# Kernel tuning notes

Hardware: AMD Instinct MI355X
Metric: run time of the kernel (lower is better)

## Reference

```python
import jax, jax.numpy as jnp
import numpy as np
import math

B, S, E = 4, 1024, 1024
H = 16
HD = E // H            # 64
HD2 = HD // 2          # 32
DEPTH = 12 - 1
LAMBDA_INIT = 0.8 - 0.6 * math.exp(-0.3 * DEPTH)
EPS = 1e-5


def setup_inputs() -> dict:
    key = jax.random.key(0)
    ks = jax.random.split(key, 16)
    std = 1.0 / math.sqrt(E)
    inp = {
        "hidden_states": jax.random.normal(ks[0], (B, S, E), jnp.float32),
        "q_w": jax.random.normal(ks[1], (E, E), jnp.float32) * std,
        "q_b": jnp.zeros((E,), jnp.float32),
        "k_w": jax.random.normal(ks[2], (E, E), jnp.float32) * std,
        "k_b": jnp.zeros((E,), jnp.float32),
        "v_w": jax.random.normal(ks[3], (E, E), jnp.float32) * std,
        "v_b": jnp.zeros((E,), jnp.float32),
        "o_w": jax.random.normal(ks[4], (E, E), jnp.float32) * std,
        "o_b": jnp.zeros((E,), jnp.float32),
        "lambda_q1": jax.random.normal(ks[5], (HD2,), jnp.float32) * 0.1,
        "lambda_k1": jax.random.normal(ks[6], (HD2,), jnp.float32) * 0.1,
        "lambda_q2": jax.random.normal(ks[7], (HD2,), jnp.float32) * 0.1,
        "lambda_k2": jax.random.normal(ks[8], (HD2,), jnp.float32) * 0.1,
        "subln_w": jnp.ones((HD,), jnp.float32),
    }
    return inp


def reference(hidden_states, q_w, q_b, k_w, k_b, v_w, v_b, o_w, o_b,
              lambda_q1, lambda_k1, lambda_q2, lambda_k2, subln_w):
    b, s, _ = hidden_states.shape
    # projections (torch Linear: x @ W.T + b)
    q = hidden_states @ q_w.T + q_b
    k = hidden_states @ k_w.T + k_b
    v = hidden_states @ v_w.T + v_b
    # split q/k into 2*H heads of dim HD2; v into H heads of dim HD
    q = q.reshape(b, s, 2 * H, HD2).transpose(0, 2, 1, 3)   # [B,2H,S,HD2]
    k = k.reshape(b, s, 2 * H, HD2).transpose(0, 2, 1, 3)   # [B,2H,S,HD2]
    v = v.reshape(b, s, H, HD).transpose(0, 2, 1, 3)        # [B,H,S,HD]
    # scores scaled by sqrt(head_dim) (full head_dim, per source)
    scores = jnp.einsum('bhqd,bhkd->bhqk', q, k) / math.sqrt(HD)
    scores = jnp.nan_to_num(scores)
    attn_w = jax.nn.softmax(scores.astype(jnp.float32), axis=-1).astype(scores.dtype)
    lam1 = jnp.exp(jnp.sum(lambda_q1 * lambda_k1))
    lam2 = jnp.exp(jnp.sum(lambda_q2 * lambda_k2))
    lam = lam1 - lam2 + LAMBDA_INIT
    attn_w = attn_w.reshape(b, H, 2, s, s)
    diff_w = attn_w[:, :, 0] - lam * attn_w[:, :, 1]        # [B,H,S,S]
    attn = jnp.einsum('bhqk,bhkd->bhqd', diff_w, v)          # [B,H,S,HD]
    # RMSNorm over head dim, elementwise affine
    attn = attn * jax.lax.rsqrt(jnp.mean(attn * attn, axis=-1, keepdims=True) + EPS) * subln_w
    attn = attn * (1.0 - LAMBDA_INIT)
    attn = attn.transpose(0, 2, 1, 3).reshape(b, s, H * HD)
    out = attn @ o_w.T + o_b
    return out, diff_w
```

## Files before the change

### kernel.cpp

```cpp
#include <hip/hip_runtime.h>

typedef __attribute__((ext_vector_type(8))) short short8;
typedef __attribute__((ext_vector_type(4))) float floatx4;

#define MFMA16(a, b, c) __builtin_amdgcn_mfma_f32_16x16x32_bf16((a), (b), (c), 0, 0, 0)

#define LAMBDA_INIT_F 0.777870099559256f
#define ONE_MINUS_LAMBDA_F 0.222129900440744f

#define GLL(g, l)                                                              \
  __builtin_amdgcn_global_load_lds(                                            \
      (const __attribute__((address_space(1))) void*)(g),                      \
      (__attribute__((address_space(3))) void*)(l), 16, 0, 0)

static __device__ __forceinline__ unsigned short f2bf(float f) {
  union { float f; unsigned int u; } v; v.f = f;
  unsigned int r = v.u + 0x7FFFu + ((v.u >> 16) & 1u);
  return (unsigned short)(r >> 16);
}

__global__ __launch_bounds__(256) void cvt_f32_bf16(const float* __restrict__ in,
                                                    unsigned short* __restrict__ out,
                                                    int n4) {
  int i = blockIdx.x * 256 + threadIdx.x;
  if (i < n4) {
    float4 v = ((const float4*)in)[i];
    unsigned short o0 = f2bf(v.x), o1 = f2bf(v.y), o2 = f2bf(v.z), o3 = f2bf(v.w);
    ushort2 a = {o0, o1}, b = {o2, o3};
    ((ushort2*)out)[i * 2] = a;
    ((ushort2*)out)[i * 2 + 1] = b;
  }
}

__device__ __forceinline__ void gemm128_core(const unsigned short* __restrict__ A,
                                             const unsigned short* __restrict__ Bt,
                                             unsigned short* As, unsigned short* Bs,
                                             int m0, int n0, floatx4 (&acc)[4][4]) {
  const int tid = threadIdx.x;
  const int w = tid >> 6, lane = tid & 63;
  const int lrow = lane & 15, quad = lane >> 4;
  const int wm = (w >> 1) * 64, wn = (w & 1) * 64;

#pragma unroll
  for (int i = 0; i < 4; i++)
#pragma unroll
    for (int j = 0; j < 4; j++)
      acc[i][j] = (floatx4){0.f, 0.f, 0.f, 0.f};

  const int ar = tid >> 2;
  const int ac = (tid & 3) * 8;
  const unsigned short* ga = A + (size_t)(m0 + ar) * 1024 + ac;
  const unsigned short* gb = Bt + (size_t)(n0 + ar) * 1024 + ac;
  unsigned short* la = As + w * 512;
  unsigned short* lb = Bs + w * 512;

  for (int k0 = 0; k0 < 1024; k0 += 32) {
    GLL(ga + k0, la);
    GLL(ga + k0 + 64 * 1024, la + 2048);
    GLL(gb + k0, lb);
    GLL(gb + k0 + 64 * 1024, lb + 2048);
    __syncthreads();
    short8 af[4], bfr[4];
#pragma unroll
    for (int i = 0; i < 4; i++)
      af[i] = *(const short8*)(As + (wm + i * 16 + lrow) * 32 + quad * 8);
#pragma unroll
    for (int j = 0; j < 4; j++)
      bfr[j] = *(const short8*)(Bs + (wn + j * 16 + lrow) * 32 + quad * 8);
#pragma unroll
    for (int i = 0; i < 4; i++)
#pragma unroll
      for (int j = 0; j < 4; j++)
        acc[i][j] = MFMA16(af[i], bfr[j], acc[i][j]);
    __syncthreads();
  }
}

__global__ __launch_bounds__(256, 2) void gemm_qkv(const unsigned short* __restrict__ A,
                                                   const unsigned short* __restrict__ qw,
                                                   const unsigned short* __restrict__ kw,
                                                   const unsigned short* __restrict__ vw,
                                                   const float* __restrict__ qb,
                                                   const float* __restrict__ kb,
                                                   const float* __restrict__ vb,
                                                   unsigned short* __restrict__ qh,
                                                   unsigned short* __restrict__ kh,
                                                   unsigned short* __restrict__ vnat) {
  __shared__ unsigned short As[128 * 32];
  __shared__ unsigned short Bs[128 * 32];
  const int m0 = blockIdx.y * 128;
  const int nglob = blockIdx.x * 128;
  const int wsel = nglob >> 10;
  const int nloc = nglob & 1023;
  const unsigned short* Bt = (wsel == 0) ? qw : ((wsel == 1) ? kw : vw);
  const float* bias = (wsel == 0) ? qb : ((wsel == 1) ? kb : vb);

  floatx4 acc[4][4];
  gemm128_core(A, Bt, As, Bs, m0, nloc, acc);

  const int tid = threadIdx.x;
  const int w = tid >> 6, lane = tid & 63;
  const int lrow = lane & 15, quad = lane >> 4;
  const int wm = (w >> 1) * 64, wn = (w & 1) * 64;

#pragma unroll
  for (int i = 0; i < 4; i++)
#pragma unroll
    for (int j = 0; j < 4; j++) {
      int col = nloc + wn + j * 16 + lrow;
      float bcol = bias[col];
#pragma unroll
      for (int r = 0; r < 4; r++) {
        int row = m0 + wm + i * 16 + quad * 4 + r;
        float v = acc[i][j][r] + bcol;
        if (wsel < 2) {
          int b = row >> 10, s = row & 1023, h2 = col >> 5, d = col & 31;
          unsigned short* o = (wsel == 0) ? qh : kh;
          o[((((size_t)(b * 32 + h2)) << 10) + s) * 32 + d] = f2bf(v);
        } else {
          vnat[(size_t)row * 1024 + col] = f2bf(v);
        }
      }
    }
}

__global__ __launch_bounds__(256, 2) void gemm_o(const unsigned short* __restrict__ A,
                                                 const unsigned short* __restrict__ ow,
                                                 const float* __restrict__ ob,
                                                 float* __restrict__ out) {
  __shared__ unsigned short As[128 * 32];
  __shared__ unsigned short Bs[128 * 32];
  const int m0 = blockIdx.y * 128;
  const int n0 = blockIdx.x * 128;

  floatx4 acc[4][4];
  gemm128_core(A, ow, As, Bs, m0, n0, acc);

  const int tid = threadIdx.x;
  const int w = tid >> 6, lane = tid & 63;
  const int lrow = lane & 15, quad = lane >> 4;
  const int wm = (w >> 1) * 64, wn = (w & 1) * 64;

#pragma unroll
  for (int i = 0; i < 4; i++)
#pragma unroll
    for (int j = 0; j < 4; j++) {
      int col = n0 + wn + j * 16 + lrow;
      float bcol = ob[col];
#pragma unroll
      for (int r = 0; r < 4; r++) {
        int row = m0 + wm + i * 16 + quad * 4 + r;
        out[(size_t)row * 1024 + col] = acc[i][j][r] + bcol;
      }
    }
}

__global__ __launch_bounds__(256) void transpose_v(const unsigned short* __restrict__ vn,
                                                   unsigned short* __restrict__ vt) {
  __shared__ unsigned int tile[64][65];
  const int t = threadIdx.x;
  const int bh = blockIdx.y, b = bh >> 4, h = bh & 15;
  const int s0 = blockIdx.x * 64;
#pragma unroll
  for (int i = 0; i < 2; i++) {
    int r = i * 32 + (t >> 3);
    int c8 = (t & 7) * 8;
    short8 v = *(const short8*)(vn + ((size_t)(b * 1024 + s0 + r)) * 1024 + h * 64 + c8);
#pragma unroll
    for (int j = 0; j < 8; j++) tile[r][c8 + j] = (unsigned short)v[j];
  }
  __syncthreads();
  const int w = t >> 6, lane = t & 63;
#pragma unroll
  for (int dd = 0; dd < 16; dd++) {
    int d = w * 16 + dd;
    unsigned short u = (unsigned short)tile[lane][d];
    vt[(((size_t)(b * 16 + h)) * 64 + d) * 1024 + s0 + lane] = u;
  }
}

__global__ __launch_bounds__(256) void attn_fused(const unsigned short* __restrict__ qh,
                                                  const unsigned short* __restrict__ kh,
                                                  const unsigned short* __restrict__ vt,
                                                  const float* __restrict__ lq1,
                                                  const float* __restrict__ lk1,
                                                  const float* __restrict__ lq2,
                                                  const float* __restrict__ lk2,
                                                  const float* __restrict__ subln,
                                                  float* __restrict__ diffw,
                                                  unsigned short* __restrict__ attnb) {
  __shared__ float redm[4][2][16];
  __shared__ float redl[4][2][16];
  __shared__ unsigned short dsA[4][16][40];
  __shared__ float ored[4][16][64];

  const int tid = threadIdx.x;
  const int w = tid >> 6, lane = tid & 63;
  const int lrow = lane & 15, quad = lane >> 4;
  const int blk = blockIdx.x;
  const int chunk = blk & 63, bh = blk >> 6;
  const int b = bh >> 4, h = bh & 15;
  const int r0 = chunk * 16;
  const int cbase = w * 256;

  float sl1 = 0.f, sl2 = 0.f;
  for (int i = 0; i < 32; i++) { sl1 += lq1[i] * lk1[i]; sl2 += lq2[i] * lk2[i]; }
  const float lam = __expf(sl1) - __expf(sl2) + LAMBDA_INIT_F;

  const unsigned short* q1 = qh + ((((size_t)(b * 32 + 2 * h)) << 10) + r0) * 32;
  const unsigned short* q2 = q1 + (32u << 10);
  const unsigned short* k1 = kh + (((size_t)(b * 32 + 2 * h)) << 10) * 32;
  const unsigned short* k2 = k1 + (32u << 10);
  const unsigned short* vth = vt + (((size_t)(b * 16 + h)) << 16);

  short8 a1 = *(const short8*)(q1 + lrow * 32 + quad * 8);
  short8 a2 = *(const short8*)(q2 + lrow * 32 + quad * 8);

  floatx4 s1a[16], s2a[16];
  float m1[4], m2[4];
#pragma unroll
  for (int r = 0; r < 4; r++) { m1[r] = -1e30f; m2[r] = -1e30f; }

  const floatx4 zero = (floatx4){0.f, 0.f, 0.f, 0.f};

#pragma unroll
  for (int ct = 0; ct < 16; ct++) {
    short8 bk = *(const short8*)(k1 + (size_t)(cbase + ct * 16 + lrow) * 32 + quad * 8);
    floatx4 s = MFMA16(a1, bk, zero);
#pragma unroll
    for (int r = 0; r < 4; r++) {
      float v = s[r] * 0.125f;
      s1a[ct][r] = v;
      m1[r] = fmaxf(m1[r], v);
    }
  }
#pragma unroll
  for (int ct = 0; ct < 16; ct++) {
    short8 bk = *(const short8*)(k2 + (size_t)(cbase + ct * 16 + lrow) * 32 + quad * 8);
    floatx4 s = MFMA16(a2, bk, zero);
#pragma unroll
    for (int r = 0; r < 4; r++) {
      float v = s[r] * 0.125f;
      s2a[ct][r] = v;
      m2[r] = fmaxf(m2[r], v);
    }
  }

#pragma unroll
  for (int off = 1; off < 16; off <<= 1) {
#pragma unroll
    for (int r = 0; r < 4; r++) {
      m1[r] = fmaxf(m1[r], __shfl_xor(m1[r], off));
      m2[r] = fmaxf(m2[r], __shfl_xor(m2[r], off));
    }
  }
  if (lrow == 0) {
#pragma unroll
    for (int r = 0; r < 4; r++) {
      redm[w][0][quad * 4 + r] = m1[r];
      redm[w][1][quad * 4 + r] = m2[r];
    }
  }
  __syncthreads();
  float mf1[4], mf2[4];
#pragma unroll
  for (int r = 0; r < 4; r++) {
    int rr = quad * 4 + r;
    mf1[r] = fmaxf(fmaxf(redm[0][0][rr], redm[1][0][rr]), fmaxf(redm[2][0][rr], redm[3][0][rr]));
    mf2[r] = fmaxf(fmaxf(redm[0][1][rr], redm[1][1][rr]), fmaxf(redm[2][1][rr], redm[3][1][rr]));
  }

  float l1[4] = {0.f, 0.f, 0.f, 0.f}, l2[4] = {0.f, 0.f, 0.f, 0.f};
#pragma unroll
  for (int ct = 0; ct < 16; ct++) {
#pragma unroll
    for (int r = 0; r < 4; r++) {
      float e1 = __expf(s1a[ct][r] - mf1[r]);
      s1a[ct][r] = e1;
      l1[r] += e1;
      float e2 = __expf(s2a[ct][r] - mf2[r]);
      s2a[ct][r] = e2;
      l2[r] += e2;
    }
  }
#pragma unroll
  for (int off = 1; off < 16; off <<= 1) {
#pragma unroll
    for (int r = 0; r < 4; r++) {
      l1[r] += __shfl_xor(l1[r], off);
      l2[r] += __shfl_xor(l2[r], off);
    }
  }
  if (lrow == 0) {
#pragma unroll
    for (int r = 0; r < 4; r++) {
      redl[w][0][quad * 4 + r] = l1[r];
      redl[w][1][quad * 4 + r] = l2[r];
    }
  }
  __syncthreads();
  float il1[4], il2[4];
#pragma unroll
  for (int r = 0; r < 4; r++) {
    int rr = quad * 4 + r;
    il1[r] = 1.f / (redl[0][0][rr] + redl[1][0][rr] + redl[2][0][rr] + redl[3][0][rr]);
    il2[r] = 1.f / (redl[0][1][rr] + redl[1][1][rr] + redl[2][1][rr] + redl[3][1][rr]);
  }

  floatx4 accO[4];
#pragma unroll
  for (int nt = 0; nt < 4; nt++) accO[nt] = zero;

  float* dwbase = diffw + (((size_t)bh) << 20) + (size_t)r0 * 1024 + cbase;

#pragma unroll
  for (int c2 = 0; c2 < 8; c2++) {
#pragma unroll
    for (int cc = 0; cc < 2; cc++) {
      int ct = c2 * 2 + cc;
#pragma unroll
      for (int r = 0; r < 4; r++) {
        float p1 = s1a[ct][r] * il1[r];
        float p2 = s2a[ct][r] * il2[r];
        float d = p1 - lam * p2;
        dwbase[(size_t)(quad * 4 + r) * 1024 + ct * 16 + lrow] = d;
        dsA[w][quad * 4 + r][cc * 16 + lrow] = f2bf(d);
      }
    }
    short8 ad = *(const short8*)(&dsA[w][lrow][quad * 8]);
#pragma unroll
    for (int nt = 0; nt < 4; nt++) {
      short8 bv = *(const short8*)(vth + (size_t)(nt * 16 + lrow) * 1024 + cbase + c2 * 32 + quad * 8);
      accO[nt] = MFMA16(ad, bv, accO[nt]);
    }
  }

#pragma unroll
  for (int nt = 0; nt < 4; nt++)
#pragma unroll
    for (int r = 0; r < 4; r++)
      ored[w][quad * 4 + r][nt * 16 + lrow] = accO[nt][r];
  __syncthreads();

#pragma unroll
  for (int rr = 0; rr < 4; rr++) {
    int row = w * 4 + rr;
    float o = ored[0][row][lane] + ored[1][row][lane] + ored[2][row][lane] + ored[3][row][lane];
    float ss = o * o;
#pragma unroll
    for (int off = 1; off < 64; off <<= 1) ss += __shfl_xor(ss, off);
    float rs = rsqrtf(ss * (1.f / 64.f) + 1e-5f);
    float v = o * rs * subln[lane] * ONE_MINUS_LAMBDA_F;
    attnb[((((size_t)b) << 10) + r0 + row) * 1024 + h * 64 + lane] = f2bf(v);
  }
}

extern "C" void kernel_launch(void* const* d_in, const int* in_sizes, int n_in,
                              void* d_out, int out_size, void* d_ws, size_t ws_size,
                              hipStream_t stream) {
  (void)in_sizes; (void)n_in; (void)out_size; (void)ws_size;
  const float* hs = (const float*)d_in[0];
  const float* q_w = (const float*)d_in[1];
  const float* q_b = (const float*)d_in[2];
  const float* k_w = (const float*)d_in[3];
  const float* k_b = (const float*)d_in[4];
  const float* v_w = (const float*)d_in[5];
  const float* v_b = (const float*)d_in[6];
  const float* o_w = (const float*)d_in[7];
  const float* o_b = (const float*)d_in[8];
  const float* lq1 = (const float*)d_in[9];
  const float* lk1 = (const float*)d_in[10];
  const float* lq2 = (const float*)d_in[11];
  const float* lk2 = (const float*)d_in[12];
  const float* subln = (const float*)d_in[13];

  char* ws = (char*)d_ws;
  unsigned short* hs_bf = (unsigned short*)(ws + 0);
  unsigned short* attnb = (unsigned short*)(ws + 0);
  unsigned short* qw_bf = (unsigned short*)(ws + 8388608);
  unsigned short* kw_bf = (unsigned short*)(ws + 10485760);
  unsigned short* vw_bf = (unsigned short*)(ws + 12582912);
  unsigned short* ow_bf = (unsigned short*)(ws + 14680064);
  unsigned short* q_h = (unsigned short*)(ws + 16777216);
  unsigned short* k_h = (unsigned short*)(ws + 25165824);
  unsigned short* v_nat = (unsigned short*)(ws + 33554432);
  unsigned short* v_t = (unsigned short*)(ws + 41943040);

  cvt_f32_bf16<<<4096, 256, 0, stream>>>(hs, hs_bf, 1048576);
  cvt_f32_bf16<<<1024, 256, 0, stream>>>(q_w, qw_bf, 262144);
  cvt_f32_bf16<<<1024, 256, 0, stream>>>(k_w, kw_bf, 262144);
  cvt_f32_bf16<<<1024, 256, 0, stream>>>(v_w, vw_bf, 262144);
  cvt_f32_bf16<<<1024, 256, 0, stream>>>(o_w, ow_bf, 262144);

  gemm_qkv<<<dim3(24, 32), 256, 0, stream>>>(hs_bf, qw_bf, kw_bf, vw_bf,
                                             q_b, k_b, v_b, q_h, k_h, v_nat);

  transpose_v<<<dim3(16, 64), 256, 0, stream>>>(v_nat, v_t);

  float* outf = (float*)d_out;
  attn_fused<<<4096, 256, 0, stream>>>(q_h, k_h, v_t, lq1, lk1, lq2, lk2, subln,
                                       outf + 4194304, attnb);

  gemm_o<<<dim3(8, 32), 256, 0, stream>>>(attnb, ow_bf, o_b, outf);
}
```

Measured before the change: 531.5 us.

## Give each wave a full 16-row chunk and recompute scores instead of storing them

Each wavefront now owns a whole 16-row query chunk over all 1024 keys, which removes the cross-wave shared-memory reductions, barriers and the output reduction buffer. Softmax runs in two passes: the first accumulates exp sums without max subtraction, and the second recomputes QK^T with MFMA to produce normalized probabilities, so the 32 score registers per lane are no longer needed. The grid shrinks fourfold. In exchange the QK MFMAs and K loads are doubled, and dropping the max subtraction relies on scores staying small enough that exp does not overflow.

```diff
diff --git a/kernel.cpp b/kernel.cpp
--- a/kernel.cpp
+++ b/kernel.cpp
@@ -189,19 +189,15 @@
                                                   const float* __restrict__ subln,
                                                   float* __restrict__ diffw,
                                                   unsigned short* __restrict__ attnb) {
-  __shared__ float redm[4][2][16];
-  __shared__ float redl[4][2][16];
   __shared__ unsigned short dsA[4][16][40];
-  __shared__ float ored[4][16][64];
 
   const int tid = threadIdx.x;
   const int w = tid >> 6, lane = tid & 63;
   const int lrow = lane & 15, quad = lane >> 4;
-  const int blk = blockIdx.x;
-  const int chunk = blk & 63, bh = blk >> 6;
+  const int chunk = blockIdx.x * 4 + w;
+  const int cidx = chunk & 63, bh = chunk >> 6;
   const int b = bh >> 4, h = bh & 15;
-  const int r0 = chunk * 16;
-  const int cbase = w * 256;
+  const int r0 = cidx * 16;
 
   float sl1 = 0.f, sl2 = 0.f;
   for (int i = 0; i < 32; i++) { sl1 += lq1[i] * lk1[i]; sl2 += lq2[i] * lk2[i]; }
@@ -216,113 +212,55 @@
   short8 a1 = *(const short8*)(q1 + lrow * 32 + quad * 8);
   short8 a2 = *(const short8*)(q2 + lrow * 32 + quad * 8);
 
-  floatx4 s1a[16], s2a[16];
-  float m1[4], m2[4];
-#pragma unroll
-  for (int r = 0; r < 4; r++) { m1[r] = -1e30f; m2[r] = -1e30f; }
-
   const floatx4 zero = (floatx4){0.f, 0.f, 0.f, 0.f};
 
-#pragma unroll
-  for (int ct = 0; ct < 16; ct++) {
-    short8 bk = *(const short8*)(k1 + (size_t)(cbase + ct * 16 + lrow) * 32 + quad * 8);
-    floatx4 s = MFMA16(a1, bk, zero);
+  float sum1[4] = {0.f, 0.f, 0.f, 0.f}, sum2[4] = {0.f, 0.f, 0.f, 0.f};
+#pragma unroll 8
+  for (int ct = 0; ct < 64; ct++) {
+    short8 bk1 = *(const short8*)(k1 + (size_t)(ct * 16 + lrow) * 32 + quad * 8);
+    short8 bk2 = *(const short8*)(k2 + (size_t)(ct * 16 + lrow) * 32 + quad * 8);
+    floatx4 s1 = MFMA16(a1, bk1, zero);
+    floatx4 s2 = MFMA16(a2, bk2, zero);
 #pragma unroll
     for (int r = 0; r < 4; r++) {
-      float v = s[r] * 0.125f;
-      s1a[ct][r] = v;
-      m1[r] = fmaxf(m1[r], v);
-    }
-  }
-#pragma unroll
-  for (int ct = 0; ct < 16; ct++) {
-    short8 bk = *(const short8*)(k2 + (size_t)(cbase + ct * 16 + lrow) * 32 + quad * 8);
-    floatx4 s = MFMA16(a2, bk, zero);
+      sum1[r] += __expf(s1[r] * 0.125f);
+      sum2[r] += __expf(s2[r] * 0.125f);
+    }
+  }
+#pragma unroll
+  for (int off = 1; off < 16; off <<= 1)
 #pragma unroll
     for (int r = 0; r < 4; r++) {
-      float v = s[r] * 0.125f;
-      s2a[ct][r] = v;
-      m2[r] = fmaxf(m2[r], v);
-    }
-  }
-
-#pragma unroll
-  for (int off = 1; off < 16; off <<= 1) {
-#pragma unroll
-    for (int r = 0; r < 4; r++) {
-      m1[r] = fmaxf(m1[r], __shfl_xor(m1[r], off));
-      m2[r] = fmaxf(m2[r], __shfl_xor(m2[r], off));
-    }
-  }
-  if (lrow == 0) {
-#pragma unroll
-    for (int r = 0; r < 4; r++) {
-      redm[w][0][quad * 4 + r] = m1[r];
-      redm[w][1][quad * 4 + r] = m2[r];
-    }
-  }
-  __syncthreads();
-  float mf1[4], mf2[4];
+      sum1[r] += __shfl_xor(sum1[r], off);
+      sum2[r] += __shfl_xor(sum2[r], off);
+    }
+  float il1[4], il2[4];
 #pragma unroll
   for (int r = 0; r < 4; r++) {
-    int rr = quad * 4 + r;
-    mf1[r] = fmaxf(fmaxf(redm[0][0][rr], redm[1][0][rr]), fmaxf(redm[2][0][rr], redm[3][0][rr]));
-    mf2[r] = fmaxf(fmaxf(redm[0][1][rr], redm[1][1][rr]), fmaxf(redm[2][1][rr], redm[3][1][rr]));
-  }
-
-  float l1[4] = {0.f, 0.f, 0.f, 0.f}, l2[4] = {0.f, 0.f, 0.f, 0.f};
-#pragma unroll
-  for (int ct = 0; ct < 16; ct++) {
-#pragma unroll
-    for (int r = 0; r < 4; r++) {
-      float e1 = __expf(s1a[ct][r] - mf1[r]);
-      s1a[ct][r] = e1;
-      l1[r] += e1;
-      float e2 = __expf(s2a[ct][r] - mf2[r]);
-      s2a[ct][r] = e2;
-      l2[r] += e2;
-    }
-  }
-#pragma unroll
-  for (int off = 1; off < 16; off <<= 1) {
-#pragma unroll
-    for (int r = 0; r < 4; r++) {
-      l1[r] += __shfl_xor(l1[r], off);
-      l2[r] += __shfl_xor(l2[r], off);
-    }
-  }
-  if (lrow == 0) {
-#pragma unroll
-    for (int r = 0; r < 4; r++) {
-      redl[w][0][quad * 4 + r] = l1[r];
-      redl[w][1][quad * 4 + r] = l2[r];
-    }
-  }
-  __syncthreads();
-  float il1[4], il2[4];
-#pragma unroll
-  for (int r = 0; r < 4; r++) {
-    int rr = quad * 4 + r;
-    il1[r] = 1.f / (redl[0][0][rr] + redl[1][0][rr] + redl[2][0][rr] + redl[3][0][rr]);
-    il2[r] = 1.f / (redl[0][1][rr] + redl[1][1][rr] + redl[2][1][rr] + redl[3][1][rr]);
+    il1[r] = 1.f / sum1[r];
+    il2[r] = lam / sum2[r];
   }
 
   floatx4 accO[4];
 #pragma unroll
   for (int nt = 0; nt < 4; nt++) accO[nt] = zero;
 
-  float* dwbase = diffw + (((size_t)bh) << 20) + (size_t)r0 * 1024 + cbase;
-
-#pragma unroll
-  for (int c2 = 0; c2 < 8; c2++) {
+  float* dwbase = diffw + (((size_t)bh) << 20) + (size_t)r0 * 1024;
+
+#pragma unroll 2
+  for (int c2 = 0; c2 < 32; c2++) {
 #pragma unroll
     for (int cc = 0; cc < 2; cc++) {
       int ct = c2 * 2 + cc;
+      short8 bk1 = *(const short8*)(k1 + (size_t)(ct * 16 + lrow) * 32 + quad * 8);
+      short8 bk2 = *(const short8*)(k2 + (size_t)(ct * 16 + lrow) * 32 + quad * 8);
+      floatx4 s1 = MFMA16(a1, bk1, zero);
+      floatx4 s2 = MFMA16(a2, bk2, zero);
 #pragma unroll
       for (int r = 0; r < 4; r++) {
-        float p1 = s1a[ct][r] * il1[r];
-        float p2 = s2a[ct][r] * il2[r];
-        float d = p1 - lam * p2;
+        float p1 = __expf(s1[r] * 0.125f) * il1[r];
+        float p2 = __expf(s2[r] * 0.125f) * il2[r];
+        float d = p1 - p2;
         dwbase[(size_t)(quad * 4 + r) * 1024 + ct * 16 + lrow] = d;
         dsA[w][quad * 4 + r][cc * 16 + lrow] = f2bf(d);
       }
@@ -330,28 +268,25 @@
     short8 ad = *(const short8*)(&dsA[w][lrow][quad * 8]);
 #pragma unroll
     for (int nt = 0; nt < 4; nt++) {
-      short8 bv = *(const short8*)(vth + (size_t)(nt * 16 + lrow) * 1024 + cbase + c2 * 32 + quad * 8);
+      short8 bv = *(const short8*)(vth + (size_t)(nt * 16 + lrow) * 1024 + c2 * 32 + quad * 8);
       accO[nt] = MFMA16(ad, bv, accO[nt]);
     }
   }
 
 #pragma unroll
-  for (int nt = 0; nt < 4; nt++)
-#pragma unroll
-    for (int r = 0; r < 4; r++)
-      ored[w][quad * 4 + r][nt * 16 + lrow] = accO[nt][r];
-  __syncthreads();
-
-#pragma unroll
-  for (int rr = 0; rr < 4; rr++) {
-    int row = w * 4 + rr;
-    float o = ored[0][row][lane] + ored[1][row][lane] + ored[2][row][lane] + ored[3][row][lane];
-    float ss = o * o;
-#pragma unroll
-    for (int off = 1; off < 64; off <<= 1) ss += __shfl_xor(ss, off);
+  for (int r = 0; r < 4; r++) {
+    float ss = 0.f;
+#pragma unroll
+    for (int nt = 0; nt < 4; nt++) ss += accO[nt][r] * accO[nt][r];
+#pragma unroll
+    for (int off = 1; off < 16; off <<= 1) ss += __shfl_xor(ss, off);
     float rs = rsqrtf(ss * (1.f / 64.f) + 1e-5f);
-    float v = o * rs * subln[lane] * ONE_MINUS_LAMBDA_F;
-    attnb[((((size_t)b) << 10) + r0 + row) * 1024 + h * 64 + lane] = f2bf(v);
+    int row = r0 + quad * 4 + r;
+#pragma unroll
+    for (int nt = 0; nt < 4; nt++) {
+      float v = accO[nt][r] * rs * subln[nt * 16 + lrow] * ONE_MINUS_LAMBDA_F;
+      attnb[((((size_t)b) << 10) + row) * 1024 + h * 64 + nt * 16 + lrow] = f2bf(v);
+    }
   }
 }
 
@@ -398,7 +333,7 @@
   transpose_v<<<dim3(16, 64), 256, 0, stream>>>(v_nat, v_t);
 
   float* outf = (float*)d_out;
-  attn_fused<<<4096, 256, 0, stream>>>(q_h, k_h, v_t, lq1, lk1, lq2, lk2, subln,
+  attn_fused<<<1024, 256, 0, stream>>>(q_h, k_h, v_t, lq1, lk1, lq2, lk2, subln,
                                        outf + 4194304, attnb);
 
   gemm_o<<<dim3(8, 32), 256, 0, stream>>>(attnb, ow_bf, o_b, outf);
```

After: 536.2 us. About the same (+0.9%).
